# Performance work log

Hardware: AMD Instinct MI355X
Metric: run time of the kernel (lower is better)

Reference implementation:

```python
import jax, jax.numpy as jnp
import numpy as np

B, N, M, D, V = 16, 2048, 2048, 128, 128


def setup_inputs() -> dict:
    key0 = jax.random.key(0)
    kq, kk, kv, kp = jax.random.split(key0, 4)
    return {
        "query": jax.random.normal(kq, (B, N, D), dtype=jnp.float32),
        "key": jax.random.normal(kk, (B, M, D), dtype=jnp.float32),
        "value": jax.random.normal(kv, (B, M, V), dtype=jnp.float32),
        "key_padding_len": jax.random.randint(kp, (B,), 0, 512),
        "is_attn_mask_len": 1,  # Python int -> causal masking on
    }


def reference(query, key, value, key_padding_len, is_attn_mask_len):
    # query:[B,N,D], key:[B,M,D], value:[B,M,V], key_padding_len:[B]
    Bq, Nq, Dq = query.shape
    Mk = key.shape[1]
    scale = 1.0 / jnp.sqrt(jnp.asarray(Dq, dtype=query.dtype))

    # torch mask(): zero out the LAST key_padding_len key positions
    pos = jnp.arange(Mk)
    keep = pos[None, :] < (Mk - key_padding_len)[:, None]  # [B,M]
    key = jnp.where(keep[:, :, None], key, jnp.zeros((), key.dtype))

    score = jnp.einsum("bnd,bmd->bnm", query, key) * scale  # [B,N,M]

    if is_attn_mask_len:
        # attn_mask_len[b,i] = M-1-i  ->  row i keeps positions j <= i (causal)
        causal = pos[None, :] <= jnp.arange(Nq)[:, None]  # [N,M]
        score = jnp.where(causal[None, :, :], score, jnp.asarray(-1e6, score.dtype))

    attn = jax.nn.softmax(score, axis=-1)  # dropout p=0 -> identity
    out = jnp.einsum("bnm,bmv->bnv", attn, value)  # [B,N,V]
    return out
```

## Files before the change

kernel.cpp:

```cpp
#include <hip/hip_runtime.h>
#include <stdint.h>

typedef unsigned short ushort_t;
typedef __attribute__((ext_vector_type(8))) short short8;
typedef __attribute__((ext_vector_type(4))) float floatx4;

#define SEQ_N 2048
#define SEQ_M 2048
#define DIM_D 128
#define DIM_V 128
#define BC 64


#if __has_builtin(__builtin_amdgcn_exp2f)
#define EXP2F(x) __builtin_amdgcn_exp2f(x)
#else
#define EXP2F(x) exp2f(x)
#endif

template <int CTRL>
__device__ __forceinline__ float dpp_f(float x) {
  int xi = __builtin_bit_cast(int, x);
  int yi = __builtin_amdgcn_update_dpp(xi, xi, CTRL, 0xf, 0xf, false);
  return __builtin_bit_cast(float, yi);
}
__device__ __forceinline__ float rowmax16(float x) {
  x = fmaxf(x, dpp_f<0x128>(x));
  x = fmaxf(x, dpp_f<0x124>(x));
  x = fmaxf(x, dpp_f<0x122>(x));
  x = fmaxf(x, dpp_f<0x121>(x));
  return x;
}
__device__ __forceinline__ float rowsum16(float x) {
  x += dpp_f<0x128>(x);
  x += dpp_f<0x124>(x);
  x += dpp_f<0x122>(x);
  x += dpp_f<0x121>(x);
  return x;
}

__device__ __forceinline__ ushort_t f2bf(float f) {
  uint32_t u = __builtin_bit_cast(uint32_t, f);
  return (ushort_t)((u + 0x8000u) >> 16);
}
__device__ __forceinline__ uint32_t bfpack(float lo, float hi) {
  uint32_t a = __builtin_bit_cast(uint32_t, lo) + 0x8000u;
  uint32_t b = __builtin_bit_cast(uint32_t, hi) + 0x8000u;
  return __builtin_amdgcn_perm(b, a, 0x07060302u);
}

#define BM2 128
#define K2OFF 0
#define V2OFF 16384
#define P2OFF 32768
#define SMEM2 40960
#define KELEMS 8192
#define VELEMS 8192

#define WS2_KB 0
#define WS2_VT 2097152
#define WS2_PO 4194304
#define WS2_M  8388608
#define WS2_L  8454144
#define WS2_FLOATS 8519680

__device__ __forceinline__ void stage16(const ushort_t* src, ushort_t* lds_base, int lane) {
#if __has_builtin(__builtin_amdgcn_global_load_lds)
  __builtin_amdgcn_global_load_lds(
      (const __attribute__((address_space(1))) void*)src,
      (__attribute__((address_space(3))) void*)lds_base, 16, 0, 0);
#else
  *(uint4*)(lds_base + lane * 8) = *(const uint4*)src;
#endif
}

__global__ __launch_bounds__(256)
void prep2(const float* __restrict__ K, const float* __restrict__ Vg,
           const int* __restrict__ kpl, float* __restrict__ ws) {
  __shared__ __align__(16) ushort_t lt[64][72];
  ushort_t* Kb = (ushort_t*)(ws + WS2_KB);
  ushort_t* Vt = (ushort_t*)(ws + WS2_VT);
  const int g = blockIdx.x, tid = threadIdx.x;
  if (g < 2048) {
    const size_t e = (size_t)g * 2048 + (size_t)tid * 8;
    const int row = (int)(e >> 7);
    const int b = row >> 11, mm = row & 2047;
    const int mlimit = SEQ_M - kpl[b];
    uint4 kw = make_uint4(0u, 0u, 0u, 0u);
    if (mm < mlimit) {
      const float* p = K + e;
      float4 f0 = *(const float4*)p, f1 = *(const float4*)(p + 4);
      kw.x = bfpack(f0.x, f0.y); kw.y = bfpack(f0.z, f0.w);
      kw.z = bfpack(f1.x, f1.y); kw.w = bfpack(f1.z, f1.w);
    }
    *(uint4*)(Kb + e) = kw;
  } else {
    const int g2 = g - 2048;
    const int b = g2 >> 6;
    const int mt = (g2 & 63) >> 1;
    const int vh = (g2 & 1) * 64;
    const int mrow = tid >> 2, v0 = (tid & 3) * 16;
    const float* p = Vg + ((size_t)b * SEQ_M + (size_t)(mt * 64 + mrow)) * DIM_V + vh + v0;
    float4 f0 = *(const float4*)p, f1 = *(const float4*)(p + 4);
    float4 f2 = *(const float4*)(p + 8), f3 = *(const float4*)(p + 12);
    lt[v0 +  0][mrow] = f2bf(f0.x); lt[v0 +  1][mrow] = f2bf(f0.y);
    lt[v0 +  2][mrow] = f2bf(f0.z); lt[v0 +  3][mrow] = f2bf(f0.w);
    lt[v0 +  4][mrow] = f2bf(f1.x); lt[v0 +  5][mrow] = f2bf(f1.y);
    lt[v0 +  6][mrow] = f2bf(f1.z); lt[v0 +  7][mrow] = f2bf(f1.w);
    lt[v0 +  8][mrow] = f2bf(f2.x); lt[v0 +  9][mrow] = f2bf(f2.y);
    lt[v0 + 10][mrow] = f2bf(f2.z); lt[v0 + 11][mrow] = f2bf(f2.w);
    lt[v0 + 12][mrow] = f2bf(f3.x); lt[v0 + 13][mrow] = f2bf(f3.y);
    lt[v0 + 14][mrow] = f2bf(f3.z); lt[v0 + 15][mrow] = f2bf(f3.w);
    __syncthreads();
    const int v = tid >> 2, mo = (tid & 3) * 16;
    ushort_t* dst = Vt + ((size_t)(b * DIM_V + vh + v) * SEQ_M) + mt * 64 + mo;
    *(uint4*)(dst + 0) = *(const uint4*)&lt[v][mo];
    *(uint4*)(dst + 8) = *(const uint4*)&lt[v][mo + 8];
  }
}

__global__ __launch_bounds__(512, 4)
void fa2(const float* __restrict__ Q, const int* __restrict__ amask,
         float* __restrict__ Out, float* __restrict__ ws) {
  __shared__ __align__(16) ushort_t sm[SMEM2];
  const ushort_t* __restrict__ Kb = (const ushort_t*)(ws + WS2_KB);
  const ushort_t* __restrict__ Vt = (const ushort_t*)(ws + WS2_VT);

  const int tid = threadIdx.x;
  const int lane = tid & 63;
  const int w = tid >> 6;
  const int qd = lane >> 4;
  const int nn = lane & 15;

  const int bx = blockIdx.x;
  const int xcd = bx & 7;
  const int q8 = bx >> 3;
  const int b = xcd * 2 + (q8 & 1);
  const int u = q8 >> 1;
  const int p = q8 & 1;
  const int c = (u >= 16) ? 1 : 0;
  int rt;
  if (p == 0) rt = c ? (u - 16) : (15 - u);
  else        rt = c ? (31 - u) : u;

  const int flag = amask[0];
  const int ntf = flag ? (2 * rt + 2) : (SEQ_M / BC);
  const int sp  = flag ? (rt + 1) : (SEQ_M / BC / 2);
  const int jt_lo = c ? sp : 0;
  const int jt_hi = c ? ntf : sp;

  const int i0w = rt * BM2 + w * 16;
  const float c1 = 0.08838834764831845f * 1.4426950408889634f;

  short8 qf[4];
  {
    const float* Qb = Q + ((size_t)b * SEQ_N + (size_t)(i0w + nn)) * DIM_D;
    union { short8 v; uint32_t u32[4]; } tq;
#pragma unroll
    for (int ks = 0; ks < 4; ++ks) {
      const float* pq = Qb + ks * 32 + qd * 8;
      float4 f0 = *(const float4*)pq, f1 = *(const float4*)(pq + 4);
      tq.u32[0] = bfpack(f0.x, f0.y);
      tq.u32[1] = bfpack(f0.z, f0.w);
      tq.u32[2] = bfpack(f1.x, f1.y);
      tq.u32[3] = bfpack(f1.z, f1.w);
      qf[ks] = tq.v;
    }
  }

  floatx4 o[8];
#pragma unroll
  for (int vt = 0; vt < 8; ++vt) o[vt] = (floatx4)0.0f;
  float m[4], l[4];
#pragma unroll
  for (int r = 0; r < 4; ++r) { m[r] = -3.0e38f; l[r] = 0.0f; }

  const size_t kbatch = (size_t)b * (SEQ_M * DIM_D);
  const size_t vbatch = (size_t)b * ((size_t)DIM_V * SEQ_M);

  auto stage = [&](int buf, int jt) {
    const int jb = jt * BC;
#pragma unroll
    for (int i = 0; i < 2; ++i) {
      const int seg = w + 8 * i;
      {
        const int rrow = seg * 4 + (lane >> 4);
        const int col  = (lane & 15) * 8;
        const ushort_t* src = Kb + kbatch + ((size_t)(jb + rrow) << 7)
                              + (col ^ ((rrow & 7) << 3));
        stage16(src, &sm[K2OFF + buf * KELEMS + seg * 512], lane);
      }
      {
        const int vrow = seg * 8 + (lane >> 3);
        const int col  = (lane & 7) * 8;
        const ushort_t* src = Vt + vbatch + ((size_t)vrow << 11) + jb
                              + (col ^ ((vrow & 7) << 3));
        stage16(src, &sm[V2OFF + buf * VELEMS + seg * 512], lane);
      }
    }
  };

  stage(0, jt_lo);
  __syncthreads();

  const int len = jt_hi - jt_lo;
  const int swl = (nn & 7) << 3;
#pragma unroll 1
  for (int t = 0; t < len; ++t) {
    const int cur = t & 1;
    const int jbase = (jt_lo + t) * BC;
    if (t + 1 < len) stage(cur ^ 1, jt_lo + t + 1);

    const int kb = K2OFF + cur * KELEMS;
    const int vb = V2OFF + cur * VELEMS;

    floatx4 s[4];
#pragma unroll
    for (int ct = 0; ct < 4; ++ct) s[ct] = (floatx4)0.0f;
    __builtin_amdgcn_s_setprio(1);
#pragma unroll
    for (int ks = 0; ks < 4; ++ks) {
#pragma unroll
      for (int ct = 0; ct < 4; ++ct) {
        short8 bf = *(const short8*)&sm[kb + (ct * 16 + nn) * 128
                                        + ((ks * 32 + qd * 8) ^ swl)];
        s[ct] = __builtin_amdgcn_mfma_f32_16x16x32_bf16(qf[ks], bf, s[ct], 0, 0, 0);
      }
    }
    __builtin_amdgcn_s_setprio(0);

    {
      const bool needmask = flag && (jbase + BC - 1 > i0w);
      if (needmask) {
#pragma unroll
        for (int ct = 0; ct < 4; ++ct) {
          const int jgl = jbase + ct * 16 + nn;
#pragma unroll
          for (int r = 0; r < 4; ++r) {
            float tv = s[ct][r] * c1;
            s[ct][r] = (jgl > i0w + qd * 4 + r) ? -3.0e38f : tv;
          }
        }
      } else {
#pragma unroll
        for (int ct = 0; ct < 4; ++ct)
#pragma unroll
          for (int r = 0; r < 4; ++r) s[ct][r] *= c1;
      }
#pragma unroll
      for (int r = 0; r < 4; ++r) {
        float mr = fmaxf(fmaxf(s[0][r], s[1][r]), fmaxf(s[2][r], s[3][r]));
        mr = rowmax16(mr);
        const float mn = fmaxf(m[r], mr);
        const float alpha = EXP2F(m[r] - mn);
        m[r] = mn;
        const int prow = w * 16 + qd * 4 + r;
        const int psw = ((qd * 4 + r) & 7) << 3;
        float ps = 0.0f;
#pragma unroll
        for (int ct = 0; ct < 4; ++ct) {
          float pv = EXP2F(s[ct][r] - mn);
          ps += pv;
          sm[P2OFF + prow * 64 + ((ct * 16 + nn) ^ psw)] = f2bf(pv);
        }
        l[r] = l[r] * alpha + ps;
#pragma unroll
        for (int vt = 0; vt < 8; ++vt) o[vt][r] *= alpha;
      }
    }

    __builtin_amdgcn_s_setprio(1);
#pragma unroll
    for (int ks2 = 0; ks2 < 2; ++ks2) {
      short8 a = *(const short8*)&sm[P2OFF + (w * 16 + nn) * 64
                                     + ((ks2 * 32 + qd * 8) ^ swl)];
#pragma unroll
      for (int vt = 0; vt < 8; ++vt) {
        short8 vbf = *(const short8*)&sm[vb + (vt * 16 + nn) * 64
                                         + ((ks2 * 32 + qd * 8) ^ swl)];
        o[vt] = __builtin_amdgcn_mfma_f32_16x16x32_bf16(a, vbf, o[vt], 0, 0, 0);
      }
    }
    __builtin_amdgcn_s_setprio(0);

    __syncthreads();
  }

#pragma unroll
  for (int r = 0; r < 4; ++r) l[r] = rowsum16(l[r]);

  const int rb = b * 16 + rt;
  if (c == 0) {
    float* Od = Out + ((size_t)b * SEQ_N + i0w) * DIM_V;
#pragma unroll
    for (int r = 0; r < 4; ++r) {
      const int row = qd * 4 + r;
#pragma unroll
      for (int vt = 0; vt < 8; ++vt)
        Od[(size_t)row * DIM_V + vt * 16 + nn] = o[vt][r];
    }
  } else {
    float* Od = ws + WS2_PO + (size_t)rb * (BM2 * DIM_V);
#pragma unroll
    for (int r = 0; r < 4; ++r) {
      const int row = w * 16 + qd * 4 + r;
#pragma unroll
      for (int vt = 0; vt < 8; ++vt)
        Od[(size_t)row * DIM_V + vt * 16 + nn] = o[vt][r];
    }
  }
  if (nn == 0) {
    const int slot = rb * 2 + c;
#pragma unroll
    for (int r = 0; r < 4; ++r) {
      const int row = w * 16 + qd * 4 + r;
      ws[WS2_M + slot * 128 + row] = m[r];
      ws[WS2_L + slot * 128 + row] = l[r];
    }
  }
}

__global__ __launch_bounds__(256)
void fa2_merge(float* __restrict__ Out, const float* __restrict__ ws) {
  const int w = threadIdx.x >> 6, lane = threadIdx.x & 63;
  const int rowid = blockIdx.x * 4 + w;
  const int rb = rowid >> 7, rr = rowid & 127;
  const int b = rb >> 4, rt = rb & 15;
  const float m1 = ws[WS2_M + (rb * 2 + 0) * 128 + rr];
  const float l1 = ws[WS2_L + (rb * 2 + 0) * 128 + rr];
  const float m2 = ws[WS2_M + (rb * 2 + 1) * 128 + rr];
  const float l2 = ws[WS2_L + (rb * 2 + 1) * 128 + rr];
  const float M = fmaxf(m1, m2);
  const float a1 = EXP2F(m1 - M), a2 = EXP2F(m2 - M);
  const float inv = 1.0f / (l1 * a1 + l2 * a2);
  float* O1 = Out + ((size_t)b * SEQ_N + (size_t)rt * BM2 + rr) * DIM_V;
  const float* O2 = ws + WS2_PO + ((size_t)rb * (BM2 * DIM_V) + (size_t)rr * DIM_V);
  float2 x1 = *(const float2*)(O1 + lane * 2);
  float2 x2 = *(const float2*)(O2 + lane * 2);
  float2 r;
  r.x = (x1.x * a1 + x2.x * a2) * inv;
  r.y = (x1.y * a1 + x2.y * a2) * inv;
  *(float2*)(O1 + lane * 2) = r;
}


#define KS_LD 136
#define VS_LD 72
#define PS_LD 72
#define KB(i) ((i) * 8704)
#define VB(i) (17408 + (i) * 9216)
#define P0 35840
#define SMEM_ELEMS 40448

#define WS_O_FLOATS (256 * 2 * 64 * 128)
#define WS_M_OFF    WS_O_FLOATS
#define WS_L_OFF    (WS_O_FLOATS + 32768)
#define WS_FLOATS   (WS_O_FLOATS + 65536)

__device__ __forceinline__ void process_chunk(
    const float* __restrict__ Q, const float* __restrict__ K,
    const float* __restrict__ Vg, float* __restrict__ Out,
    float* __restrict__ ws, ushort_t* __restrict__ smem,
    int b, int rt, int jt_lo, int jt_hi, int mlimit, int flag, int c, bool direct) {
  const int tid  = threadIdx.x;
  const int lane = tid & 63;
  const int w    = tid >> 6;
  const int qd   = lane >> 4;
  const int nn   = lane & 15;

  const float c1 = 0.08838834764831845f * 1.4426950408889634f;

  const int oct = tid & 15;
  const int j0  = (tid >> 4) * 4;
  const int hh  = nn >> 3;
  const int rb  = 8 * hh;

  const int i0w = rt * 64 + w * 16;
  const size_t koff = (size_t)b * SEQ_M * DIM_D;
  const size_t voff = (size_t)b * SEQ_M * DIM_V;

  short8 qf[4];
  {
    const float* Qb = Q + ((size_t)b * SEQ_N + (size_t)(i0w + nn)) * DIM_D;
    union { short8 v; uint32_t u32[4]; } t;
#pragma unroll
    for (int ks = 0; ks < 4; ++ks) {
      const float* p = Qb + ks * 32 + qd * 8;
      float4 f0 = *(const float4*)p, f1 = *(const float4*)(p + 4);
      t.u32[0] = bfpack(f0.x, f0.y);
      t.u32[1] = bfpack(f0.z, f0.w);
      t.u32[2] = bfpack(f1.x, f1.y);
      t.u32[3] = bfpack(f1.z, f1.w);
      qf[ks] = t.v;
    }
  }

  floatx4 o[8];
#pragma unroll
  for (int vt = 0; vt < 8; ++vt) o[vt] = (floatx4)0.0f;
  float m[4], l[4];
#pragma unroll
  for (int r = 0; r < 4; ++r) { m[r] = -3.0e38f; l[r] = 0.0f; }

  float4 kr[4][2], vr[4][2];

  auto stage_load = [&](int jt) {
    const int jbase = jt * BC;
#pragma unroll
    for (int r = 0; r < 4; ++r) {
      const float* kp = K  + koff + (size_t)(jbase + j0 + r) * DIM_D + oct * 8;
      kr[r][0] = *(const float4*)kp;  kr[r][1] = *(const float4*)(kp + 4);
      const float* vp = Vg + voff + (size_t)(jbase + j0 + r) * DIM_V + oct * 8;
      vr[r][0] = *(const float4*)vp;  vr[r][1] = *(const float4*)(vp + 4);
    }
  };

  auto stage_write = [&](int buf, int jt) {
    const int jbase = jt * BC;
    const int kb = KB(buf), vb = VB(buf);
#pragma unroll
    for (int r = 0; r < 4; ++r) {
      uint4 kw;
      kw.x = bfpack(kr[r][0].x, kr[r][0].y);
      kw.y = bfpack(kr[r][0].z, kr[r][0].w);
      kw.z = bfpack(kr[r][1].x, kr[r][1].y);
      kw.w = bfpack(kr[r][1].z, kr[r][1].w);
      if (jbase + j0 + r >= mlimit) kw = make_uint4(0u, 0u, 0u, 0u);
      *(uint4*)(smem + kb + (j0 + r) * KS_LD + oct * 8) = kw;
    }
    float vc[4][8];
#pragma unroll
    for (int r = 0; r < 4; ++r) {
      vc[r][0]=vr[r][0].x; vc[r][1]=vr[r][0].y; vc[r][2]=vr[r][0].z; vc[r][3]=vr[r][0].w;
      vc[r][4]=vr[r][1].x; vc[r][5]=vr[r][1].y; vc[r][6]=vr[r][1].z; vc[r][7]=vr[r][1].w;
    }
#pragma unroll
    for (int q = 0; q < 8; ++q) {
      const int p = 8 * oct + ((oct + q) & 7);
      uint2 dv;
      dv.x = bfpack(vc[0][q], vc[1][q]);
      dv.y = bfpack(vc[2][q], vc[3][q]);
      *(uint2*)(smem + vb + p * VS_LD + j0) = dv;
    }
  };

  stage_load(jt_lo);
  stage_write(0, jt_lo);
  __syncthreads();

  const int len = jt_hi - jt_lo;
#pragma unroll 1
  for (int t = 0; t < len; ++t) {
    const int jt = jt_lo + t;
    const int cur = t & 1;
    const bool more = (t + 1) < len;
    const int jbase = jt * BC;
    if (more) stage_load(jt + 1);

    const int kb = KB(cur), vb = VB(cur);

    floatx4 s[4];
#pragma unroll
    for (int ct = 0; ct < 4; ++ct) s[ct] = (floatx4)0.0f;
#pragma unroll
    for (int ks = 0; ks < 4; ++ks) {
#pragma unroll
      for (int ct = 0; ct < 4; ++ct) {
        short8 bf = *(const short8*)(smem + kb + (ct * 16 + nn) * KS_LD + ks * 32 + qd * 8);
        s[ct] = __builtin_amdgcn_mfma_f32_16x16x32_bf16(qf[ks], bf, s[ct], 0, 0, 0);
      }
    }

    {
      float tt[4][4];
      const bool needmask = flag && (jbase + BC - 1 > i0w);
#pragma unroll
      for (int ct = 0; ct < 4; ++ct)
#pragma unroll
        for (int r = 0; r < 4; ++r) {
          float tv = s[ct][r] * c1;
          if (needmask) {
            int jgl = jbase + ct * 16 + nn;
            int igl = i0w + qd * 4 + r;
            if (jgl > igl) tv = -3.0e38f;
          }
          tt[ct][r] = tv;
        }
#pragma unroll
      for (int r = 0; r < 4; ++r) {
        float mr = fmaxf(fmaxf(tt[0][r], tt[1][r]), fmaxf(tt[2][r], tt[3][r]));
        mr = rowmax16(mr);
        float mn = fmaxf(m[r], mr);
        float alpha = EXP2F(m[r] - mn);
        m[r] = mn;
        float ps = 0.0f;
#pragma unroll
        for (int ct = 0; ct < 4; ++ct) {
          float p = EXP2F(tt[ct][r] - mn);
          tt[ct][r] = p;
          ps += p;
        }
        l[r] = l[r] * alpha + ps;
#pragma unroll
        for (int vt = 0; vt < 8; ++vt) o[vt][r] *= alpha;
      }
#pragma unroll
      for (int ct = 0; ct < 4; ++ct)
#pragma unroll
        for (int r = 0; r < 4; ++r)
          smem[P0 + (w * 16 + qd * 4 + r) * PS_LD + ct * 16 + nn] = f2bf(tt[ct][r]);
    }

#pragma unroll
    for (int ks2 = 0; ks2 < 2; ++ks2) {
      short8 a = *(const short8*)(smem + P0 + (w * 16 + nn) * PS_LD + ks2 * 32 + qd * 8);
#pragma unroll
      for (int vt = 0; vt < 8; ++vt) {
        const int p = 16 * vt + rb + ((2 * vt + nn + hh) & 7);
        short8 vbf = *(const short8*)(smem + vb + p * VS_LD + ks2 * 32 + qd * 8);
        o[vt] = __builtin_amdgcn_mfma_f32_16x16x32_bf16(a, vbf, o[vt], 0, 0, 0);
      }
    }

    if (more) stage_write(cur ^ 1, jt + 1);
    __syncthreads();
  }

#pragma unroll
  for (int r = 0; r < 4; ++r) l[r] = rowsum16(l[r]);

  if (direct) {
    float* Ob = Out + ((size_t)b * SEQ_N + i0w) * DIM_V;
#pragma unroll
    for (int r = 0; r < 4; ++r) {
      float inv = 1.0f / l[r];
      int row = qd * 4 + r;
#pragma unroll
      for (int vt = 0; vt < 8; ++vt)
        Ob[(size_t)row * DIM_V + vt * 16 + nn] = o[vt][r] * inv;
    }
  } else {
    const int p = b * 16 + (rt - 16);
    const int slot = p * 2 + c;
    float* Op = ws + (size_t)slot * 64 * 128;
#pragma unroll
    for (int r = 0; r < 4; ++r) {
      int row = w * 16 + qd * 4 + r;
#pragma unroll
      for (int vt = 0; vt < 8; ++vt)
        Op[(size_t)row * 128 + vt * 16 + nn] = o[vt][r];
    }
    if (nn == 0) {
#pragma unroll
      for (int r = 0; r < 4; ++r) {
        int row = w * 16 + qd * 4 + r;
        ws[WS_M_OFF + slot * 64 + row] = m[r];
        ws[WS_L_OFF + slot * 64 + row] = l[r];
      }
    }
  }
}

__global__ __launch_bounds__(256, 2)
void fa_chunk(const float* __restrict__ Q, const float* __restrict__ K,
              const float* __restrict__ Vg, const int* __restrict__ kpl,
              const int* __restrict__ amask, float* __restrict__ Out,
              float* __restrict__ ws) {
  __shared__ __align__(16) ushort_t smem[SMEM_ELEMS];
  const int bx = blockIdx.x;
  const int b  = bx & 15;
  const int u  = bx >> 4;
  int rt, c;
  if (u < 16)      { rt = 16 + u; c = 0; }
  else if (u < 32) { rt = 47 - u; c = 1; }
  else             { rt = 47 - u; c = 0; }
  const int flag   = amask[0];
  const int mlimit = SEQ_M - kpl[b];
  const int ntiles = flag ? (rt + 1) : (SEQ_M / BC);
  const int jt_lo  = (c == 1) ? 16 : 0;
  const int jt_hi  = (c == 0 && rt >= 16) ? 16 : ntiles;
  process_chunk(Q, K, Vg, Out, ws, smem, b, rt, jt_lo, jt_hi, mlimit, flag, c, rt < 16);
}

__global__ __launch_bounds__(256)
void fa_merge(const float* __restrict__ ws, float* __restrict__ Out) {
  const int w = threadIdx.x >> 6, lane = threadIdx.x & 63;
  const int rowid = blockIdx.x * 4 + w;
  const int p = rowid >> 6, rr = rowid & 63;
  const int b = p >> 4, rt = 16 + (p & 15);
  float m1 = ws[WS_M_OFF + (p * 2 + 0) * 64 + rr];
  float l1 = ws[WS_L_OFF + (p * 2 + 0) * 64 + rr];
  float m2 = ws[WS_M_OFF + (p * 2 + 1) * 64 + rr];
  float l2 = ws[WS_L_OFF + (p * 2 + 1) * 64 + rr];
  float M  = fmaxf(m1, m2);
  float a1 = EXP2F(m1 - M), a2 = EXP2F(m2 - M);
  float inv = 1.0f / (l1 * a1 + l2 * a2);
  const float* O1 = ws + ((size_t)(p * 2 + 0) * 64 + rr) * 128;
  const float* O2 = ws + ((size_t)(p * 2 + 1) * 64 + rr) * 128;
  float2 x1 = *(const float2*)(O1 + lane * 2);
  float2 x2 = *(const float2*)(O2 + lane * 2);
  float2 r;
  r.x = (x1.x * a1 + x2.x * a2) * inv;
  r.y = (x1.y * a1 + x2.y * a2) * inv;
  *(float2*)(Out + ((size_t)b * SEQ_N + rt * 64 + rr) * 128 + lane * 2) = r;
}

__global__ __launch_bounds__(256, 2)
void fa_paired(const float* __restrict__ Q, const float* __restrict__ K,
               const float* __restrict__ Vg, const int* __restrict__ kpl,
               const int* __restrict__ amask, float* __restrict__ Out) {
  __shared__ __align__(16) ushort_t smem[SMEM_ELEMS];
  const int bx = blockIdx.x;
  const int b  = bx & 15;
  const int pp = bx >> 4;
  const int flag   = amask[0];
  const int mlimit = SEQ_M - kpl[b];
#pragma unroll 1
  for (int ph = 0; ph < 2; ++ph) {
    const int rt = ph ? (31 - pp) : pp;
    const int ntiles = flag ? (rt + 1) : (SEQ_M / BC);
    process_chunk(Q, K, Vg, Out, nullptr, smem, b, rt, 0, ntiles, mlimit, flag, 0, true);
  }
}

extern "C" void kernel_launch(void* const* d_in, const int* in_sizes, int n_in,
                              void* d_out, int out_size, void* d_ws, size_t ws_size,
                              hipStream_t stream) {
  const float* Q   = (const float*)d_in[0];
  const float* K   = (const float*)d_in[1];
  const float* V   = (const float*)d_in[2];
  const int* kpl   = (const int*)d_in[3];
  const int* amask = (const int*)d_in[4];
  float* O         = (float*)d_out;
  float* ws        = (float*)d_ws;

  if (ws_size >= (size_t)WS2_FLOATS * 4) {
    hipLaunchKernelGGL(prep2, dim3(3072), dim3(256), 0, stream, K, V, kpl, ws);
    hipLaunchKernelGGL(fa2, dim3(512), dim3(512), 0, stream, Q, amask, O, ws);
    hipLaunchKernelGGL(fa2_merge, dim3(8192), dim3(256), 0, stream, O, ws);
  } else if (ws_size >= (size_t)WS_FLOATS * 4) {
    hipLaunchKernelGGL(fa_chunk, dim3(768), dim3(256), 0, stream, Q, K, V, kpl, amask, O, ws);
    hipLaunchKernelGGL(fa_merge, dim3(4096), dim3(256), 0, stream, ws, O);
  } else {
    hipLaunchKernelGGL(fa_paired, dim3(256), dim3(256), 0, stream, Q, K, V, kpl, amask, O);
  }
}
```

Before: 161.7 us.

## Shrink fa2 tiles to 64 query rows and 32 keys with lazy rescaling

The main attention kernel moves from 128-row query tiles with 512 threads and 64-key steps to 64-row tiles with 256 threads and 32-key steps. This doubles the block count and halves LDS per block, which is meant to improve occupancy and load balance under causal masking. The block-to-(batch, row-tile, split) mapping and the LDS swizzles for V and P are redone, and the merge kernel is updated to match. It also adds a lazy rescale that updates the running max and rescales the accumulators only when the new row max exceeds the old by more than 8 in log2 units. The lazy rescale cuts exp and multiply work, at the cost of more loop iterations and more K/V reloads per output row.

```diff
diff --git a/kernel.cpp b/kernel.cpp
--- a/kernel.cpp
+++ b/kernel.cpp
@@ -10,6 +10,7 @@
 #define DIM_D 128
 #define DIM_V 128
 #define BC 64
+#define BC2 32
 
 
 #if __has_builtin(__builtin_amdgcn_exp2f)
@@ -49,13 +50,12 @@
   return __builtin_amdgcn_perm(b, a, 0x07060302u);
 }
 
-#define BM2 128
 #define K2OFF 0
-#define V2OFF 16384
-#define P2OFF 32768
-#define SMEM2 40960
-#define KELEMS 8192
-#define VELEMS 8192
+#define V2OFF 8192
+#define P2OFF 16384
+#define SMEM2 18432
+#define KELEMS 4096
+#define VELEMS 4096
 
 #define WS2_KB 0
 #define WS2_VT 2097152
@@ -119,7 +119,7 @@
   }
 }
 
-__global__ __launch_bounds__(512, 4)
+__global__ __launch_bounds__(256, 4)
 void fa2(const float* __restrict__ Q, const int* __restrict__ amask,
          float* __restrict__ Out, float* __restrict__ ws) {
   __shared__ __align__(16) ushort_t sm[SMEM2];
@@ -135,21 +135,25 @@
   const int bx = blockIdx.x;
   const int xcd = bx & 7;
   const int q8 = bx >> 3;
-  const int b = xcd * 2 + (q8 & 1);
-  const int u = q8 >> 1;
-  const int p = q8 & 1;
-  const int c = (u >= 16) ? 1 : 0;
-  int rt;
-  if (p == 0) rt = c ? (u - 16) : (15 - u);
-  else        rt = c ? (31 - u) : u;
+  const int s  = q8 >> 5;
+  const int v  = q8 & 31;
+  const int p  = v & 1;
+  const int j  = v >> 1;
+  const int b  = xcd * 2 + p;
+  const int jj = p ? (15 - j) : j;
+  int rt, c;
+  if (s == 0)      { rt = jj;      c = 0; }
+  else if (s == 1) { rt = 31 - jj; c = 0; }
+  else if (s == 2) { rt = 16 + jj; c = 1; }
+  else             { rt = 15 - jj; c = 1; }
 
   const int flag = amask[0];
-  const int ntf = flag ? (2 * rt + 2) : (SEQ_M / BC);
-  const int sp  = flag ? (rt + 1) : (SEQ_M / BC / 2);
+  const int ntf = flag ? (2 * rt + 2) : (SEQ_M / BC2);
+  const int sp  = flag ? (rt + 1) : (SEQ_M / BC2 / 2);
   const int jt_lo = c ? sp : 0;
   const int jt_hi = c ? ntf : sp;
 
-  const int i0w = rt * BM2 + w * 16;
+  const int i0w = rt * 64 + w * 16;
   const float c1 = 0.08838834764831845f * 1.4426950408889634f;
 
   short8 qf[4];
@@ -179,22 +183,20 @@
   const size_t vbatch = (size_t)b * ((size_t)DIM_V * SEQ_M);
 
   auto stage = [&](int buf, int jt) {
-    const int jb = jt * BC;
+    const int jb = jt * BC2;
 #pragma unroll
     for (int i = 0; i < 2; ++i) {
-      const int seg = w + 8 * i;
+      const int seg = w * 2 + i;
       {
         const int rrow = seg * 4 + (lane >> 4);
-        const int col  = (lane & 15) * 8;
-        const ushort_t* src = Kb + kbatch + ((size_t)(jb + rrow) << 7)
-                              + (col ^ ((rrow & 7) << 3));
+        const int col  = ((lane & 15) * 8) ^ ((rrow & 7) << 3);
+        const ushort_t* src = Kb + kbatch + ((size_t)(jb + rrow) << 7) + col;
         stage16(src, &sm[K2OFF + buf * KELEMS + seg * 512], lane);
       }
       {
-        const int vrow = seg * 8 + (lane >> 3);
-        const int col  = (lane & 7) * 8;
-        const ushort_t* src = Vt + vbatch + ((size_t)vrow << 11) + jb
-                              + (col ^ ((vrow & 7) << 3));
+        const int vrow = seg * 16 + (lane >> 2);
+        const int colg = (lane & 3) ^ ((lane >> 4) & 3);
+        const ushort_t* src = Vt + vbatch + ((size_t)vrow << 11) + jb + colg * 8;
         stage16(src, &sm[V2OFF + buf * VELEMS + seg * 512], lane);
       }
     }
@@ -205,79 +207,83 @@
 
   const int len = jt_hi - jt_lo;
   const int swl = (nn & 7) << 3;
+  const int vsw = ((nn >> 2) & 3) << 3;
 #pragma unroll 1
   for (int t = 0; t < len; ++t) {
     const int cur = t & 1;
-    const int jbase = (jt_lo + t) * BC;
+    const int jbase = (jt_lo + t) * BC2;
     if (t + 1 < len) stage(cur ^ 1, jt_lo + t + 1);
 
     const int kb = K2OFF + cur * KELEMS;
     const int vb = V2OFF + cur * VELEMS;
 
-    floatx4 s[4];
-#pragma unroll
-    for (int ct = 0; ct < 4; ++ct) s[ct] = (floatx4)0.0f;
+    floatx4 sx[2];
+#pragma unroll
+    for (int ct = 0; ct < 2; ++ct) sx[ct] = (floatx4)0.0f;
     __builtin_amdgcn_s_setprio(1);
 #pragma unroll
     for (int ks = 0; ks < 4; ++ks) {
 #pragma unroll
-      for (int ct = 0; ct < 4; ++ct) {
+      for (int ct = 0; ct < 2; ++ct) {
         short8 bf = *(const short8*)&sm[kb + (ct * 16 + nn) * 128
                                         + ((ks * 32 + qd * 8) ^ swl)];
-        s[ct] = __builtin_amdgcn_mfma_f32_16x16x32_bf16(qf[ks], bf, s[ct], 0, 0, 0);
+        sx[ct] = __builtin_amdgcn_mfma_f32_16x16x32_bf16(qf[ks], bf, sx[ct], 0, 0, 0);
       }
     }
     __builtin_amdgcn_s_setprio(0);
 
     {
-      const bool needmask = flag && (jbase + BC - 1 > i0w);
+      const bool needmask = flag && (jbase + BC2 - 1 > i0w);
       if (needmask) {
 #pragma unroll
-        for (int ct = 0; ct < 4; ++ct) {
+        for (int ct = 0; ct < 2; ++ct) {
           const int jgl = jbase + ct * 16 + nn;
 #pragma unroll
           for (int r = 0; r < 4; ++r) {
-            float tv = s[ct][r] * c1;
-            s[ct][r] = (jgl > i0w + qd * 4 + r) ? -3.0e38f : tv;
+            float tv = sx[ct][r] * c1;
+            sx[ct][r] = (jgl > i0w + qd * 4 + r) ? -3.0e38f : tv;
           }
         }
       } else {
 #pragma unroll
-        for (int ct = 0; ct < 4; ++ct)
-#pragma unroll
-          for (int r = 0; r < 4; ++r) s[ct][r] *= c1;
+        for (int ct = 0; ct < 2; ++ct)
+#pragma unroll
+          for (int r = 0; r < 4; ++r) sx[ct][r] *= c1;
+      }
+      float mr4[4];
+#pragma unroll
+      for (int r = 0; r < 4; ++r) mr4[r] = rowmax16(fmaxf(sx[0][r], sx[1][r]));
+      bool need = false;
+#pragma unroll
+      for (int r = 0; r < 4; ++r) need = need || (mr4[r] > m[r] + 8.0f);
+      if (__any(need ? 1 : 0)) {
+#pragma unroll
+        for (int r = 0; r < 4; ++r) {
+          const float mn = fmaxf(m[r], mr4[r]);
+          const float alpha = EXP2F(m[r] - mn);
+          m[r] = mn;
+          l[r] *= alpha;
+#pragma unroll
+          for (int vt = 0; vt < 8; ++vt) o[vt][r] *= alpha;
+        }
       }
 #pragma unroll
       for (int r = 0; r < 4; ++r) {
-        float mr = fmaxf(fmaxf(s[0][r], s[1][r]), fmaxf(s[2][r], s[3][r]));
-        mr = rowmax16(mr);
-        const float mn = fmaxf(m[r], mr);
-        const float alpha = EXP2F(m[r] - mn);
-        m[r] = mn;
         const int prow = w * 16 + qd * 4 + r;
-        const int psw = ((qd * 4 + r) & 7) << 3;
-        float ps = 0.0f;
-#pragma unroll
-        for (int ct = 0; ct < 4; ++ct) {
-          float pv = EXP2F(s[ct][r] - mn);
-          ps += pv;
-          sm[P2OFF + prow * 64 + ((ct * 16 + nn) ^ psw)] = f2bf(pv);
-        }
-        l[r] = l[r] * alpha + ps;
-#pragma unroll
-        for (int vt = 0; vt < 8; ++vt) o[vt][r] *= alpha;
+        float p0 = EXP2F(sx[0][r] - m[r]);
+        float p1 = EXP2F(sx[1][r] - m[r]);
+        l[r] += p0 + p1;
+        sm[P2OFF + prow * 32 + ((0 * 16 + nn) ^ (qd << 3))] = f2bf(p0);
+        sm[P2OFF + prow * 32 + ((1 * 16 + nn) ^ (qd << 3))] = f2bf(p1);
       }
     }
 
     __builtin_amdgcn_s_setprio(1);
-#pragma unroll
-    for (int ks2 = 0; ks2 < 2; ++ks2) {
-      short8 a = *(const short8*)&sm[P2OFF + (w * 16 + nn) * 64
-                                     + ((ks2 * 32 + qd * 8) ^ swl)];
+    {
+      short8 a = *(const short8*)&sm[P2OFF + (w * 16 + nn) * 32 + ((qd * 8) ^ vsw)];
 #pragma unroll
       for (int vt = 0; vt < 8; ++vt) {
-        short8 vbf = *(const short8*)&sm[vb + (vt * 16 + nn) * 64
-                                         + ((ks2 * 32 + qd * 8) ^ swl)];
+        short8 vbf = *(const short8*)&sm[vb + (vt * 16 + nn) * 32 + ((qd * 8) ^ vsw)];
         o[vt] = __builtin_amdgcn_mfma_f32_16x16x32_bf16(a, vbf, o[vt], 0, 0, 0);
       }
     }
@@ -289,7 +295,7 @@
 #pragma unroll
   for (int r = 0; r < 4; ++r) l[r] = rowsum16(l[r]);
 
-  const int rb = b * 16 + rt;
+  const int rb = b * 32 + rt;
   if (c == 0) {
     float* Od = Out + ((size_t)b * SEQ_N + i0w) * DIM_V;
 #pragma unroll
@@ -300,7 +306,7 @@
         Od[(size_t)row * DIM_V + vt * 16 + nn] = o[vt][r];
     }
   } else {
-    float* Od = ws + WS2_PO + (size_t)rb * (BM2 * DIM_V);
+    float* Od = ws + WS2_PO + (size_t)rb * (64 * DIM_V);
 #pragma unroll
     for (int r = 0; r < 4; ++r) {
       const int row = w * 16 + qd * 4 + r;
@@ -314,8 +320,8 @@
 #pragma unroll
     for (int r = 0; r < 4; ++r) {
       const int row = w * 16 + qd * 4 + r;
-      ws[WS2_M + slot * 128 + row] = m[r];
-      ws[WS2_L + slot * 128 + row] = l[r];
+      ws[WS2_M + slot * 64 + row] = m[r];
+      ws[WS2_L + slot * 64 + row] = l[r];
     }
   }
 }
@@ -324,17 +330,17 @@
 void fa2_merge(float* __restrict__ Out, const float* __restrict__ ws) {
   const int w = threadIdx.x >> 6, lane = threadIdx.x & 63;
   const int rowid = blockIdx.x * 4 + w;
-  const int rb = rowid >> 7, rr = rowid & 127;
-  const int b = rb >> 4, rt = rb & 15;
-  const float m1 = ws[WS2_M + (rb * 2 + 0) * 128 + rr];
-  const float l1 = ws[WS2_L + (rb * 2 + 0) * 128 + rr];
-  const float m2 = ws[WS2_M + (rb * 2 + 1) * 128 + rr];
-  const float l2 = ws[WS2_L + (rb * 2 + 1) * 128 + rr];
+  const int rb = rowid >> 6, rr = rowid & 63;
+  const int b = rb >> 5, rt = rb & 31;
+  const float m1 = ws[WS2_M + (rb * 2 + 0) * 64 + rr];
+  const float l1 = ws[WS2_L + (rb * 2 + 0) * 64 + rr];
+  const float m2 = ws[WS2_M + (rb * 2 + 1) * 64 + rr];
+  const float l2 = ws[WS2_L + (rb * 2 + 1) * 64 + rr];
   const float M = fmaxf(m1, m2);
   const float a1 = EXP2F(m1 - M), a2 = EXP2F(m2 - M);
   const float inv = 1.0f / (l1 * a1 + l2 * a2);
-  float* O1 = Out + ((size_t)b * SEQ_N + (size_t)rt * BM2 + rr) * DIM_V;
-  const float* O2 = ws + WS2_PO + ((size_t)rb * (BM2 * DIM_V) + (size_t)rr * DIM_V);
+  float* O1 = Out + ((size_t)b * SEQ_N + (size_t)rt * 64 + rr) * DIM_V;
+  const float* O2 = ws + WS2_PO + (size_t)rb * (64 * DIM_V) + (size_t)rr * DIM_V;
   float2 x1 = *(const float2*)(O1 + lane * 2);
   float2 x2 = *(const float2*)(O2 + lane * 2);
   float2 r;
@@ -636,7 +642,7 @@
 
   if (ws_size >= (size_t)WS2_FLOATS * 4) {
     hipLaunchKernelGGL(prep2, dim3(3072), dim3(256), 0, stream, K, V, kpl, ws);
-    hipLaunchKernelGGL(fa2, dim3(512), dim3(512), 0, stream, Q, amask, O, ws);
+    hipLaunchKernelGGL(fa2, dim3(1024), dim3(256), 0, stream, Q, amask, O, ws);
     hipLaunchKernelGGL(fa2_merge, dim3(8192), dim3(256), 0, stream, O, ws);
   } else if (ws_size >= (size_t)WS_FLOATS * 4) {
     hipLaunchKernelGGL(fa_chunk, dim3(768), dim3(256), 0, stream, Q, K, V, kpl, amask, O, ws);
```

New measurement: 151.0 us. -6.6%, faster.
